# Kernel optimization log

Measured on AMD Instinct MI355X. Metric: run time of the kernel, lower is better.

The kernel has to match this reference:

```python
import jax, jax.numpy as jnp
import numpy as np
import math

EMBED = 1024
HEADS = 16
HEAD_DIM = EMBED // HEADS
FF = 4096
LAYERS = 4
BATCH = 2
SEQ = 2048
EPS = 1e-5
ADAPTIVE = True
MAX_LENGTH = 2048


def setup_inputs() -> dict:
    key = jax.random.key(0)
    ks = jax.random.split(key, 20)
    s = 0.02
    inp = {
        "x": jax.random.normal(ks[0], (BATCH, SEQ, EMBED), jnp.float32),
        # per-layer stacked parameters, torch Linear convention W:[out,in]
        "Wq": jax.random.normal(ks[1], (LAYERS, EMBED, EMBED)) * s,
        "bq": jnp.zeros((LAYERS, EMBED)),
        "Wk": jax.random.normal(ks[2], (LAYERS, EMBED, EMBED)) * s,
        "bk": jnp.zeros((LAYERS, EMBED)),
        "Wv": jax.random.normal(ks[3], (LAYERS, EMBED, EMBED)) * s,
        "bv": jnp.zeros((LAYERS, EMBED)),
        "Wo": jax.random.normal(ks[4], (LAYERS, EMBED, EMBED)) * s,
        "bo": jnp.zeros((LAYERS, EMBED)),
        "W1": jax.random.normal(ks[5], (LAYERS, FF, EMBED)) * s,
        "b1": jnp.zeros((LAYERS, FF)),
        "W2": jax.random.normal(ks[6], (LAYERS, EMBED, FF)) * s,
        "b2": jnp.zeros((LAYERS, EMBED)),
        "g1": jnp.ones((LAYERS, EMBED)),
        "be1": jnp.zeros((LAYERS, EMBED)),
        "g2": jnp.ones((LAYERS, EMBED)),
        "be2": jnp.zeros((LAYERS, EMBED)),
    }
    return inp


def _layer_norm(x, g, b):
    mu = jnp.mean(x, axis=-1, keepdims=True)
    var = jnp.mean(jnp.square(x - mu), axis=-1, keepdims=True)
    return (x - mu) * jax.lax.rsqrt(var + EPS) * g + b


def _band_mask(seq_len):
    # adaptive, length-dependent sparse band: window ~ sqrt(seq_len)
    w = int(math.ceil(math.sqrt(seq_len))) if ADAPTIVE else MAX_LENGTH
    idx = jnp.arange(seq_len)
    return jnp.abs(idx[:, None] - idx[None, :]) <= w  # [S,S] bool


def _sparse_attn(x, Wq, bq, Wk, bk, Wv, bv, Wo, bo, band):
    B, S, E = x.shape
    def proj(W, b):
        return (x @ W.T + b).reshape(B, S, HEADS, HEAD_DIM)
    q = proj(Wq, bq)
    k = proj(Wk, bk)
    v = proj(Wv, bv)
    scores = jnp.einsum("bshd,bthd->bhst", q, k) / math.sqrt(HEAD_DIM)
    scores = jnp.where(band[None, None], scores, jnp.float32(-1e9))
    attn = jax.nn.softmax(scores, axis=-1)
    out = jnp.einsum("bhst,bthd->bshd", attn, v).reshape(B, S, E)
    return out @ Wo.T + bo


def reference(x, Wq, bq, Wk, bk, Wv, bv, Wo, bo, W1, b1, W2, b2, g1, be1, g2, be2):
    band = _band_mask(x.shape[1])
    for i in range(LAYERS):
        attn = _sparse_attn(x, Wq[i], bq[i], Wk[i], bk[i], Wv[i], bv[i],
                            Wo[i], bo[i], band)
        x = _layer_norm(x + attn, g1[i], be1[i])
        ff = jax.nn.relu(x @ W1[i].T + b1[i]) @ W2[i].T + b2[i]
        x = _layer_norm(x + ff, g2[i], be2[i])
    return x  # dropout is identity in eval mode
```

## Files before the change

### kernel.cpp

```cpp
#include <hip/hip_runtime.h>
#include <hip/hip_bf16.h>

using bf16 = __hip_bfloat16;
typedef __bf16 bf16x8v __attribute__((ext_vector_type(8)));
typedef __bf16 bf16x4v __attribute__((ext_vector_type(4)));
typedef float f32x4v __attribute__((ext_vector_type(4)));

#define EMBED 1024
#define FF_DIM 4096
#define NTOK 4096
#define SEQL 2048
#define HD 64
#define WBAND 46
#define LN_EPS 1e-5f

__device__ __forceinline__ void gload16(const bf16* g, bf16* l)
{
  __builtin_amdgcn_global_load_lds(
      (const __attribute__((address_space(1))) void*)g,
      (__attribute__((address_space(3))) void*)l, 16, 0, 0);
}

__global__ __launch_bounds__(256) void detect_dtype(
    const unsigned int* __restrict__ xw, int* __restrict__ flag)
{
  __shared__ int votes[256];
  int v = 0;
#pragma unroll
  for (int j = 0; j < 4; j++) {
    unsigned int w = xw[1 + threadIdx.x * 4 + j];
    unsigned int e = (w >> 7) & 0xFFu;
    v += (e == 0u || (e >= 0x58u && e <= 0x88u)) ? 1 : 0;
  }
  votes[threadIdx.x] = v;
  __syncthreads();
  if (threadIdx.x == 0) {
    int s = 0;
    for (int i = 0; i < 256; i++) s += votes[i];
    *flag = (s > 512) ? 1 : 0;
  }
}

__global__ __launch_bounds__(256) void cast_param(
    const void* __restrict__ src, bf16* __restrict__ dst, int n,
    const int* __restrict__ dflag)
{
  const int is_bf16 = *dflag;
  for (int i = blockIdx.x * 256 + threadIdx.x; i < n; i += gridDim.x * 256)
    dst[i] = is_bf16 ? ((const bf16*)src)[i] : (bf16)(((const float*)src)[i]);
}

__global__ __launch_bounds__(256) void cast_in(
    const void* __restrict__ x, float* __restrict__ xf,
    bf16* __restrict__ xb, int n, const int* __restrict__ dflag)
{
  const int is_bf16 = *dflag;
  const int i = blockIdx.x * 256 + threadIdx.x;
  if (i < n) {
    float v = is_bf16 ? (float)((const bf16*)x)[i] : ((const float*)x)[i];
    xf[i] = v;
    xb[i] = (bf16)v;
  }
}

__global__ __launch_bounds__(256) void cast_weights(
    const void* __restrict__ wq, const void* __restrict__ wk,
    const void* __restrict__ wv, const void* __restrict__ wo,
    const void* __restrict__ w1, const void* __restrict__ w2,
    size_t off_ee, size_t off_fe, bf16* __restrict__ dst,
    const int* __restrict__ dflag)
{
  const int is_bf16 = *dflag;
  const int c = blockIdx.x * 256 + threadIdx.x;
  const size_t i = (size_t)c * 8;
  const void* src;
  size_t si;
  if (i < 4194304) {
    const int t = (int)(i >> 20);
    src = (t == 0) ? wq : (t == 1) ? wk : (t == 2) ? wv : wo;
    si  = off_ee + (i & 1048575);
  } else if (i < 8388608) { src = w1; si = off_fe + (i - 4194304); }
  else                    { src = w2; si = off_fe + (i - 8388608); }
  bf16x8v o;
  if (is_bf16) {
    o = *reinterpret_cast<const bf16x8v*>((const bf16*)src + si);
  } else {
    f32x4v a = *reinterpret_cast<const f32x4v*>((const float*)src + si);
    f32x4v b = *reinterpret_cast<const f32x4v*>((const float*)src + si + 4);
#pragma unroll
    for (int j = 0; j < 4; j++) { o[j] = (__bf16)a[j]; o[j + 4] = (__bf16)b[j]; }
  }
  *reinterpret_cast<bf16x8v*>(dst + i) = o;
}

template<int EPI, int BN>
__device__ __forceinline__ void gemm_core(
    const bf16* __restrict__ A, const bf16* __restrict__ W,
    const bf16* __restrict__ bias, bf16* __restrict__ C,
    int N, int Kstride, int Kbeg, int Klen,
    int row0, int col0W, int col0C)
{
  __shared__ __align__(16) bf16 lA[128 * 32];
  __shared__ __align__(16) bf16 lB[BN * 32];
  constexpr int NJ = BN / 32;

  const int tid  = threadIdx.x;
  const int wave = tid >> 6;
  const int lane = tid & 63;
  const int wr0  = (wave >> 1) * 64;
  const int wc0  = (wave & 1) * (BN / 2);

  f32x4v acc[4][NJ];
#pragma unroll
  for (int i = 0; i < 4; i++)
#pragma unroll
    for (int j = 0; j < NJ; j++) acc[i][j] = (f32x4v){0.f, 0.f, 0.f, 0.f};

  const int srow = wave * 16 + (lane >> 2);
  const int skc  = (lane & 3) * 8;
  const bf16* Ag = A + (size_t)(row0 + srow) * Kstride + Kbeg + skc;
  const bf16* Bg;
  if constexpr (BN == 128)
    Bg = W + (size_t)(col0W + srow) * Kstride + Kbeg + skc;
  else
    Bg = W + (size_t)(col0W + (tid >> 2)) * Kstride + Kbeg + (size_t)(tid & 3) * 8;
  bf16* lAp = lA + tid * 8;
  bf16* lBp = lB + tid * 8;

  const int fr = lane & 15;
  const int q8 = (lane >> 4) * 8;

  for (int k0 = 0; k0 < Klen; k0 += 32) {
    __syncthreads();
    gload16(Ag + k0, lAp);
    gload16(Ag + (size_t)64 * Kstride + k0, lAp + 2048);
    gload16(Bg + k0, lBp);
    if constexpr (BN == 128)
      gload16(Bg + (size_t)64 * Kstride + k0, lBp + 2048);
    __syncthreads();

    bf16x8v af[4], bw[NJ];
#pragma unroll
    for (int i = 0; i < 4; i++)
      af[i] = *reinterpret_cast<const bf16x8v*>(&lA[(wr0 + i * 16 + fr) * 32 + q8]);
#pragma unroll
    for (int j = 0; j < NJ; j++)
      bw[j] = *reinterpret_cast<const bf16x8v*>(&lB[(wc0 + j * 16 + fr) * 32 + q8]);
#pragma unroll
    for (int i = 0; i < 4; i++)
#pragma unroll
      for (int j = 0; j < NJ; j++)
        acc[i][j] = __builtin_amdgcn_mfma_f32_16x16x32_bf16(af[i], bw[j], acc[i][j], 0, 0, 0);
  }

  const int quad = (lane >> 4) * 4;
#pragma unroll
  for (int j = 0; j < NJ; j++) {
    const int col = col0C + wc0 + j * 16 + fr;
    const float bvf = bias ? (float)bias[col] : 0.f;
#pragma unroll
    for (int i = 0; i < 4; i++) {
      const int r0 = row0 + wr0 + i * 16 + quad;
#pragma unroll
      for (int r = 0; r < 4; r++) {
        float v = acc[i][j][r] + bvf;
        if (EPI == 1) v = fmaxf(v, 0.f);
        C[(size_t)(r0 + r) * N + col] = (bf16)v;
      }
    }
  }
}

template<int EPI, int BN, int NS>
__global__ __launch_bounds__(256) void gemm_bt(
    const bf16* __restrict__ A, const bf16* __restrict__ W,
    const bf16* __restrict__ bias, bf16* __restrict__ C0, bf16* __restrict__ C1,
    int N, int K)
{
  const int z  = (NS > 1) ? blockIdx.z : 0;
  const int Kp = K / NS;
  gemm_core<EPI, BN>(A, W, z == 0 ? bias : nullptr, z == 0 ? C0 : C1,
                     N, K, z * Kp, Kp,
                     blockIdx.x * 128, blockIdx.y * BN, blockIdx.y * BN);
}

__global__ __launch_bounds__(256) void gemm_qkv(
    const bf16* __restrict__ A, const bf16* __restrict__ Wqkv,
    const bf16* __restrict__ bq, const bf16* __restrict__ bk, const bf16* __restrict__ bv,
    bf16* __restrict__ Cq, bf16* __restrict__ Ck, bf16* __restrict__ Cv, int K)
{
  const int cg = blockIdx.y * 128;
  const int t  = cg >> 10;
  const bf16* bias = (t == 0) ? bq : (t == 1) ? bk : bv;
  bf16*       C    = (t == 0) ? Cq : (t == 1) ? Ck : Cv;
  gemm_core<0, 128>(A, Wqkv, bias, C, 1024, K, 0, K,
                    blockIdx.x * 128, cg, cg & 1023);
}

#define SKI(t, d)  ((((t) * 64) + (d)) ^ (((t) & 7) << 3))
#define SVI(d, t)  ((((d) * 128) + (t)) ^ (((d) & 7) << 3))
#define SPI(q, c)  ((((q) * 128) + (c)) ^ (((q) & 7) << 3))
#define SSI(q, c)  ((((q) * 128) + (c)) ^ (((q) & 7) << 2))

__global__ __launch_bounds__(256) void attn_band(
    const bf16* __restrict__ Q, const bf16* __restrict__ Kp,
    const bf16* __restrict__ Vp, bf16* __restrict__ O)
{
  const int sblk = blockIdx.x;
  const int bh   = blockIdx.y;
  const int b    = bh >> 4;
  const int h    = bh & 15;
  const int s0   = sblk * 32;
  int tlo = s0 - WBAND;       if (tlo < 0) tlo = 0;
  int thi = s0 + 31 + WBAND;  if (thi > SEQL - 1) thi = SEQL - 1;
  const int L = thi - tlo + 1;

  __shared__ __align__(16) bf16  sQf[32 * 64];
  __shared__ __align__(16) bf16  sKf[128 * 64];
  __shared__ __align__(16) bf16  sVtf[64 * 128];
  __shared__ __align__(16) float sSf[32 * 128];
  __shared__ __align__(16) bf16  sPf[32 * 128];
  __shared__ float red1[32][8];
  __shared__ float red2[32][8];
  __shared__ float sInv[32];

  const int tid  = threadIdx.x;
  const int wave = tid >> 6;
  const int lane = tid & 63;
  const size_t base = ((size_t)b * SEQL) * EMBED + (size_t)h * HD;

  bf16x8v vz;
#pragma unroll
  for (int j = 0; j < 8; j++) vz[j] = (__bf16)0.f;

  {
    const int sl = tid >> 3, d0 = (tid & 7) * 8;
    *reinterpret_cast<bf16x8v*>(&sQf[SKI(sl, d0)]) =
        *reinterpret_cast<const bf16x8v*>(&Q[base + (size_t)(s0 + sl) * EMBED + d0]);
  }
  for (int i = tid; i < 128 * 8; i += 256) {
    const int tl = i >> 3, d0 = (i & 7) * 8;
    bf16x8v v = vz;
    if (tl < L)
      v = *reinterpret_cast<const bf16x8v*>(&Kp[base + (size_t)(tlo + tl) * EMBED + d0]);
    *reinterpret_cast<bf16x8v*>(&sKf[SKI(tl, d0)]) = v;
  }
  for (int i = tid; i < 128 * 8; i += 256) {
    const int tl = i & 127, d0 = ((i >> 7) & 7) * 8;
    bf16x8v v = vz;
    if (tl < L)
      v = *reinterpret_cast<const bf16x8v*>(&Vp[base + (size_t)(tlo + tl) * EMBED + d0]);
#pragma unroll
    for (int j = 0; j < 8; j++)
      sVtf[SVI(d0 + j, tl)] = reinterpret_cast<const bf16*>(&v)[j];
  }
  __syncthreads();

  const int fr   = lane & 15;
  const int q8   = (lane >> 4) * 8;
  const int quad = (lane >> 4) * 4;

  {
    f32x4v acc[2][2];
#pragma unroll
    for (int mi = 0; mi < 2; mi++)
#pragma unroll
      for (int nj = 0; nj < 2; nj++) acc[mi][nj] = (f32x4v){0.f, 0.f, 0.f, 0.f};
#pragma unroll
    for (int ks = 0; ks < 2; ks++) {
      bf16x8v a0 = *reinterpret_cast<const bf16x8v*>(&sQf[SKI(fr,      ks * 32 + q8)]);
      bf16x8v a1 = *reinterpret_cast<const bf16x8v*>(&sQf[SKI(16 + fr, ks * 32 + q8)]);
      bf16x8v b0 = *reinterpret_cast<const bf16x8v*>(&sKf[SKI((wave * 2    ) * 16 + fr, ks * 32 + q8)]);
      bf16x8v b1 = *reinterpret_cast<const bf16x8v*>(&sKf[SKI((wave * 2 + 1) * 16 + fr, ks * 32 + q8)]);
      acc[0][0] = __builtin_amdgcn_mfma_f32_16x16x32_bf16(a0, b0, acc[0][0], 0, 0, 0);
      acc[0][1] = __builtin_amdgcn_mfma_f32_16x16x32_bf16(a0, b1, acc[0][1], 0, 0, 0);
      acc[1][0] = __builtin_amdgcn_mfma_f32_16x16x32_bf16(a1, b0, acc[1][0], 0, 0, 0);
      acc[1][1] = __builtin_amdgcn_mfma_f32_16x16x32_bf16(a1, b1, acc[1][1], 0, 0, 0);
    }
#pragma unroll
    for (int nj = 0; nj < 2; nj++) {
      const int c = (wave * 2 + nj) * 16 + fr;
      const int t = tlo + c;
      const bool cvalid = (c < L);
#pragma unroll
      for (int mi = 0; mi < 2; mi++) {
#pragma unroll
        for (int r = 0; r < 4; r++) {
          const int row = mi * 16 + quad + r;
          int dd = (s0 + row) - t; if (dd < 0) dd = -dd;
          sSf[SSI(row, c)] = (cvalid && dd <= WBAND) ? acc[mi][nj][r] * 0.125f
                                                     : -1e30f;
        }
      }
    }
  }
  __syncthreads();

  const int sl   = tid & 31;
  const int part = tid >> 5;
  float pmax = -1e30f;
#pragma unroll
  for (int k = 0; k < 16; k++) pmax = fmaxf(pmax, sSf[SSI(sl, part + 8 * k)]);
  red1[sl][part] = pmax;
  __syncthreads();
  float rmax = red1[sl][0];
#pragma unroll
  for (int p = 1; p < 8; p++) rmax = fmaxf(rmax, red1[sl][p]);

  float psum = 0.f;
#pragma unroll
  for (int k = 0; k < 16; k++) {
    const int c = part + 8 * k;
    float e = __expf(sSf[SSI(sl, c)] - rmax);
    sPf[SPI(sl, c)] = (bf16)e;
    psum += e;
  }
  red2[sl][part] = psum;
  __syncthreads();
  float rsum = 0.f;
#pragma unroll
  for (int p = 0; p < 8; p++) rsum += red2[sl][p];
  if (part == 0) sInv[sl] = 1.f / rsum;
  __syncthreads();

  {
    const int mi = wave >> 1;
    const int nb = (wave & 1) * 2;
    f32x4v acc[2];
    acc[0] = (f32x4v){0.f, 0.f, 0.f, 0.f};
    acc[1] = (f32x4v){0.f, 0.f, 0.f, 0.f};
#pragma unroll
    for (int ks = 0; ks < 4; ks++) {
      bf16x8v a  = *reinterpret_cast<const bf16x8v*>(&sPf[SPI(mi * 16 + fr, ks * 32 + q8)]);
      bf16x8v b0 = *reinterpret_cast<const bf16x8v*>(&sVtf[SVI((nb    ) * 16 + fr, ks * 32 + q8)]);
      bf16x8v b1 = *reinterpret_cast<const bf16x8v*>(&sVtf[SVI((nb + 1) * 16 + fr, ks * 32 + q8)]);
      acc[0] = __builtin_amdgcn_mfma_f32_16x16x32_bf16(a, b0, acc[0], 0, 0, 0);
      acc[1] = __builtin_amdgcn_mfma_f32_16x16x32_bf16(a, b1, acc[1], 0, 0, 0);
    }
#pragma unroll
    for (int nj = 0; nj < 2; nj++) {
      const int d = (nb + nj) * 16 + fr;
#pragma unroll
      for (int r = 0; r < 4; r++) {
        const int row = mi * 16 + quad + r;
        O[base + (size_t)(s0 + row) * EMBED + d] = (bf16)(acc[nj][r] * sInv[row]);
      }
    }
  }
}

__global__ __launch_bounds__(256) void resid_ln(
    const float* xin, const bf16* __restrict__ y0, const bf16* y1,
    const bf16* __restrict__ g, const bf16* __restrict__ be,
    float* xf_out, bf16* xb_out,
    void* __restrict__ final_out, const int* __restrict__ dflag)
{
  __shared__ float red1[4];
  __shared__ float red2[4];
  const int row = blockIdx.x;
  const int tid = threadIdx.x;
  const size_t base = (size_t)row * EMBED + (size_t)tid * 4;

  f32x4v  xv  = *reinterpret_cast<const f32x4v*>(xin + base);
  bf16x4v yv0 = *reinterpret_cast<const bf16x4v*>(y0 + base);
  bf16x4v yv1 = *reinterpret_cast<const bf16x4v*>(y1 + base);
  float v[4];
#pragma unroll
  for (int j = 0; j < 4; j++) v[j] = xv[j] + (float)yv0[j] + (float)yv1[j];

  float s = v[0] + v[1] + v[2] + v[3];
#pragma unroll
  for (int off = 32; off > 0; off >>= 1) s += __shfl_down(s, off, 64);
  if ((tid & 63) == 0) red1[tid >> 6] = s;
  __syncthreads();
  const float mu = (red1[0] + red1[1] + red1[2] + red1[3]) * (1.f / EMBED);

  float sq = 0.f;
#pragma unroll
  for (int j = 0; j < 4; j++) { const float d = v[j] - mu; sq += d * d; }
#pragma unroll
  for (int off = 32; off > 0; off >>= 1) sq += __shfl_down(sq, off, 64);
  if ((tid & 63) == 0) red2[tid >> 6] = sq;
  __syncthreads();
  const float rstd = rsqrtf((red2[0] + red2[1] + red2[2] + red2[3]) * (1.f / EMBED) + LN_EPS);

  bf16x4v gv = *reinterpret_cast<const bf16x4v*>(g + (size_t)tid * 4);
  bf16x4v bv = *reinterpret_cast<const bf16x4v*>(be + (size_t)tid * 4);
  f32x4v of;
  bf16x4v ov;
#pragma unroll
  for (int j = 0; j < 4; j++) {
    of[j] = (v[j] - mu) * rstd * (float)gv[j] + (float)bv[j];
    ov[j] = (__bf16)of[j];
  }
  *reinterpret_cast<f32x4v*>(xf_out + base) = of;
  *reinterpret_cast<bf16x4v*>(xb_out + base) = ov;
  if (final_out) {
    if (*dflag)
      *reinterpret_cast<bf16x4v*>((bf16*)final_out + base) = ov;
    else
      *reinterpret_cast<f32x4v*>((float*)final_out + base) = of;
  }
}

extern "C" void kernel_launch(void* const* d_in, const int* in_sizes, int n_in,
                              void* d_out, int out_size, void* d_ws, size_t ws_size,
                              hipStream_t stream)
{
  char* ws = (char*)d_ws;
  const size_t MB = 1024 * 1024;
  int*   flag = (int*)ws;
  bf16*  pp   = (bf16*)(ws + 4096);
  float* xf   = (float*)(ws + 1 * MB);
  bf16*  xb   = (bf16*)(ws + 17 * MB);
  bf16*  q    = (bf16*)(ws + 25 * MB);
  bf16*  kk   = (bf16*)(ws + 33 * MB);
  bf16*  vv   = (bf16*)(ws + 41 * MB);
  bf16*  ao   = q;
  bf16*  hh   = (bf16*)(ws + 25 * MB);
  bf16*  y    = (bf16*)(ws + 57 * MB);
  bf16*  wbf  = (bf16*)(ws + 65 * MB);

  bf16* pbq = pp;            bf16* pbk = pp + 4096;  bf16* pbv = pp + 8192;
  bf16* pbo = pp + 12288;    bf16* pb1 = pp + 16384; bf16* pb2 = pp + 32768;
  bf16* pg1 = pp + 36864;    bf16* pe1 = pp + 40960;
  bf16* pg2 = pp + 45056;    bf16* pe2 = pp + 49152;

  detect_dtype<<<1, 256, 0, stream>>>((const unsigned int*)d_in[0], flag);

  cast_param<<<16, 256, 0, stream>>>(d_in[2],  pbq, 4096,  flag);
  cast_param<<<16, 256, 0, stream>>>(d_in[4],  pbk, 4096,  flag);
  cast_param<<<16, 256, 0, stream>>>(d_in[6],  pbv, 4096,  flag);
  cast_param<<<16, 256, 0, stream>>>(d_in[8],  pbo, 4096,  flag);
  cast_param<<<64, 256, 0, stream>>>(d_in[10], pb1, 16384, flag);
  cast_param<<<16, 256, 0, stream>>>(d_in[12], pb2, 4096,  flag);
  cast_param<<<16, 256, 0, stream>>>(d_in[13], pg1, 4096,  flag);
  cast_param<<<16, 256, 0, stream>>>(d_in[14], pe1, 4096,  flag);
  cast_param<<<16, 256, 0, stream>>>(d_in[15], pg2, 4096,  flag);
  cast_param<<<16, 256, 0, stream>>>(d_in[16], pe2, 4096,  flag);

  cast_in<<<dim3((NTOK * EMBED) / 256), 256, 0, stream>>>(
      d_in[0], xf, xb, NTOK * EMBED, flag);

  for (int l = 0; l < 4; l++) {
    cast_weights<<<6144, 256, 0, stream>>>(
        d_in[1], d_in[3], d_in[5], d_in[7], d_in[9], d_in[11],
        (size_t)l * 1048576, (size_t)l * 4194304, wbf, flag);

    gemm_qkv<<<dim3(32, 24), 256, 0, stream>>>(
        xb, wbf, pbq + l * 1024, pbk + l * 1024, pbv + l * 1024,
        q, kk, vv, EMBED);
    attn_band<<<dim3(SEQL / 32, 32), 256, 0, stream>>>(q, kk, vv, ao);
    gemm_bt<0, 64, 2><<<dim3(32, 16, 2), 256, 0, stream>>>(
        ao, wbf + 3 * 1048576, pbo + l * 1024, kk, vv, EMBED, EMBED);
    resid_ln<<<dim3(NTOK), 256, 0, stream>>>(
        xf, kk, vv, pg1 + l * 1024, pe1 + l * 1024, xf, xb, nullptr, flag);
    gemm_bt<1, 128, 1><<<dim3(32, 32, 1), 256, 0, stream>>>(
        xb, wbf + 4 * 1048576, pb1 + l * 4096, hh, nullptr, FF_DIM, EMBED);
    gemm_bt<0, 64, 2><<<dim3(32, 16, 2), 256, 0, stream>>>(
        hh, wbf + 8 * 1048576, pb2 + l * 1024, y, xb, EMBED, FF_DIM);
    resid_ln<<<dim3(NTOK), 256, 0, stream>>>(
        xf, y, xb, pg2 + l * 1024, pe2 + l * 1024, xf, xb,
        l == 3 ? d_out : nullptr, flag);
  }
}
```

Baseline: 1.132 ms.

## Double K-step per barrier and stage GEMM epilogue through swizzled LDS

The GEMM main loop now loads 64 K-elements per iteration as two 32-wide LDS sub-tiles, halving the number of barrier pairs per tile. The epilogue writes accumulators into a swizzled shared-memory tile and then stores 16-byte vectors coalesced to global memory, replacing scattered 2-byte stores. This adds LDS usage, which may reduce occupancy, plus an extra barrier and LDS round trip in the epilogue.

```diff
diff --git a/kernel.cpp b/kernel.cpp
--- a/kernel.cpp
+++ b/kernel.cpp
@@ -93,6 +93,8 @@
   *reinterpret_cast<bf16x8v*>(dst + i) = o;
 }
 
+#define SWZ(row) ((((row) >> 2) & 7) << 3)
+
 template<int EPI, int BN>
 __device__ __forceinline__ void gemm_core(
     const bf16* __restrict__ A, const bf16* __restrict__ W,
@@ -100,9 +102,12 @@
     int N, int Kstride, int Kbeg, int Klen,
     int row0, int col0W, int col0C)
 {
-  __shared__ __align__(16) bf16 lA[128 * 32];
-  __shared__ __align__(16) bf16 lB[BN * 32];
-  constexpr int NJ = BN / 32;
+  constexpr int NJ    = BN / 32;
+  constexpr int STAGE = 128 * 64 + BN * 64;
+  constexpr int TOT   = (STAGE > 128 * BN) ? STAGE : 128 * BN;
+  __shared__ __align__(16) bf16 smem[TOT];
+  bf16* lA = smem;
+  bf16* lB = smem + 128 * 64;
 
   const int tid  = threadIdx.x;
   const int wave = tid >> 6;
@@ -116,58 +121,78 @@
 #pragma unroll
     for (int j = 0; j < NJ; j++) acc[i][j] = (f32x4v){0.f, 0.f, 0.f, 0.f};
 
-  const int srow = wave * 16 + (lane >> 2);
-  const int skc  = (lane & 3) * 8;
-  const bf16* Ag = A + (size_t)(row0 + srow) * Kstride + Kbeg + skc;
-  const bf16* Bg;
-  if constexpr (BN == 128)
-    Bg = W + (size_t)(col0W + srow) * Kstride + Kbeg + skc;
-  else
-    Bg = W + (size_t)(col0W + (tid >> 2)) * Kstride + Kbeg + (size_t)(tid & 3) * 8;
+  const int rowa = tid >> 2;
+  const int kca  = (tid & 3) * 8;
+  const bf16* Ag = A + (size_t)(row0 + rowa) * Kstride + Kbeg + kca;
+  const bf16* Bg = W + (size_t)(col0W + rowa) * Kstride + Kbeg + kca;
   bf16* lAp = lA + tid * 8;
   bf16* lBp = lB + tid * 8;
 
   const int fr = lane & 15;
   const int q8 = (lane >> 4) * 8;
 
-  for (int k0 = 0; k0 < Klen; k0 += 32) {
+  for (int k0 = 0; k0 < Klen; k0 += 64) {
     __syncthreads();
-    gload16(Ag + k0, lAp);
-    gload16(Ag + (size_t)64 * Kstride + k0, lAp + 2048);
-    gload16(Bg + k0, lBp);
-    if constexpr (BN == 128)
-      gload16(Bg + (size_t)64 * Kstride + k0, lBp + 2048);
+#pragma unroll
+    for (int h = 0; h < 2; h++) {
+#pragma unroll
+      for (int rb = 0; rb < 2; rb++)
+        gload16(Ag + (size_t)rb * 64 * Kstride + k0 + h * 32,
+                lAp + h * 4096 + rb * 2048);
+#pragma unroll
+      for (int rb = 0; rb < BN / 64; rb++)
+        gload16(Bg + (size_t)rb * 64 * Kstride + k0 + h * 32,
+                lBp + h * (BN * 32) + rb * 2048);
+    }
     __syncthreads();
 
-    bf16x8v af[4], bw[NJ];
-#pragma unroll
-    for (int i = 0; i < 4; i++)
-      af[i] = *reinterpret_cast<const bf16x8v*>(&lA[(wr0 + i * 16 + fr) * 32 + q8]);
-#pragma unroll
-    for (int j = 0; j < NJ; j++)
-      bw[j] = *reinterpret_cast<const bf16x8v*>(&lB[(wc0 + j * 16 + fr) * 32 + q8]);
-#pragma unroll
-    for (int i = 0; i < 4; i++)
+#pragma unroll
+    for (int ks = 0; ks < 2; ks++) {
+      bf16x8v af[4], bw[NJ];
+#pragma unroll
+      for (int i = 0; i < 4; i++)
+        af[i] = *reinterpret_cast<const bf16x8v*>(
+            &lA[ks * 4096 + (wr0 + i * 16 + fr) * 32 + q8]);
 #pragma unroll
       for (int j = 0; j < NJ; j++)
-        acc[i][j] = __builtin_amdgcn_mfma_f32_16x16x32_bf16(af[i], bw[j], acc[i][j], 0, 0, 0);
+        bw[j] = *reinterpret_cast<const bf16x8v*>(
+            &lB[ks * (BN * 32) + (wc0 + j * 16 + fr) * 32 + q8]);
+#pragma unroll
+      for (int i = 0; i < 4; i++)
+#pragma unroll
+        for (int j = 0; j < NJ; j++)
+          acc[i][j] = __builtin_amdgcn_mfma_f32_16x16x32_bf16(af[i], bw[j], acc[i][j], 0, 0, 0);
+    }
   }
 
   const int quad = (lane >> 4) * 4;
+  __syncthreads();
 #pragma unroll
   for (int j = 0; j < NJ; j++) {
-    const int col = col0C + wc0 + j * 16 + fr;
-    const float bvf = bias ? (float)bias[col] : 0.f;
+    const int col = wc0 + j * 16 + fr;
+    const float bvf = bias ? (float)bias[col0C + col] : 0.f;
 #pragma unroll
     for (int i = 0; i < 4; i++) {
-      const int r0 = row0 + wr0 + i * 16 + quad;
 #pragma unroll
       for (int r = 0; r < 4; r++) {
+        const int row = wr0 + i * 16 + quad + r;
         float v = acc[i][j][r] + bvf;
         if (EPI == 1) v = fmaxf(v, 0.f);
-        C[(size_t)(r0 + r) * N + col] = (bf16)v;
+        smem[row * BN + (col ^ SWZ(row))] = (bf16)v;
       }
     }
+  }
+  __syncthreads();
+  constexpr int CPR = BN / 8;
+  constexpr int RPP = 256 / CPR;
+  const int erow = tid / CPR;
+  const int ec8  = (tid % CPR) * 8;
+#pragma unroll
+  for (int p = 0; p < 128 / RPP; p++) {
+    const int row = p * RPP + erow;
+    bf16x8v v = *reinterpret_cast<const bf16x8v*>(
+        &smem[row * BN + (ec8 ^ SWZ(row))]);
+    *reinterpret_cast<bf16x8v*>(&C[(size_t)(row0 + row) * N + col0C + ec8]) = v;
   }
 }
 
```

Result: faster. 1.074 ms (-5.2%).
